# Optimization experiments

Measured on AMD Instinct MI355X. Metric: run time of the kernel, lower is better.

The kernel has to match this reference:

```python
import jax, jax.numpy as jnp
import numpy as np

B, D, C, OUT = 16384, 784, 2048, 10

def setup_inputs() -> dict:
    key = jax.random.key(0)
    k1, k2, k3 = jax.random.split(key, 3)
    x = jax.random.normal(k1, (B, D), dtype=jnp.float32)
    centres = jax.random.normal(k2, (C, D), dtype=jnp.float32)
    log_sigmas = jnp.zeros((C,), dtype=jnp.float32)
    W = jax.random.normal(k3, (OUT, C), dtype=jnp.float32) * (1.0 / np.sqrt(C))
    b = jnp.zeros((OUT,), dtype=jnp.float32)
    return {"x": x, "centres": centres, "log_sigmas": log_sigmas, "W": W, "b": b}

def reference(x, centres, log_sigmas, W, b):
    # (B, C, D) broadcast tensor the torch code materializes; same math).
    x2 = jnp.sum(x * x, axis=-1, keepdims=True)          # (B, 1)
    c2 = jnp.sum(centres * centres, axis=-1)             # (C,)
    d2 = jnp.maximum(x2 + c2[None, :] - 2.0 * (x @ centres.T), 0.0)  # (B, C)
    distances = jnp.sqrt(d2) / jnp.exp(log_sigmas)[None, :]          # (B, C)
    phi = jnp.exp(-(distances * distances))              # gaussian basis
    return phi @ W.T + b                                  # (B, OUT)
```

## Files before the change

kernel.cpp:

```cpp
#include <hip/hip_runtime.h>


#define B_ROWS 16384
#define D_DIM  784
#define C_DIM  2048
#define NOUT   10
#define KPAD   832
#define NT32   26

typedef __attribute__((ext_vector_type(8))) __bf16 bf16x8;
typedef __attribute__((ext_vector_type(4))) float  f32x4;
typedef __attribute__((ext_vector_type(4))) unsigned short ushort4v;

__device__ __forceinline__ unsigned short f2bf(float f) {
  union { float f; unsigned int u; } v; v.f = f;
  unsigned int u = v.u;
  return (unsigned short)((u + 0x7fffu + ((u >> 16) & 1u)) >> 16);
}

__device__ __forceinline__ void async16(const unsigned short* g, unsigned short* l) {
  __builtin_amdgcn_global_load_lds((const __attribute__((address_space(1))) void*)g,
                                   (__attribute__((address_space(3))) void*)l,
                                   16, 0, 0);
}

__device__ __forceinline__ void conv_row(const float* __restrict__ src,
                                         unsigned short* __restrict__ dst,
                                         float* __restrict__ sq, int row, int lane) {
  const float* s = src + (size_t)row * D_DIM;
  unsigned short* d = dst + (size_t)row * KPAD;
  float acc = 0.f;
#pragma unroll
  for (int c = 0; c < 4; ++c) {
    const int ch = lane + c * 64;
    if (ch < 196) {
      const float4 v = ((const float4*)s)[ch];
      ushort4v o; o.x = f2bf(v.x); o.y = f2bf(v.y); o.z = f2bf(v.z); o.w = f2bf(v.w);
      *(ushort4v*)(d + ch * 4) = o;
      acc += v.x * v.x + v.y * v.y + v.z * v.z + v.w * v.w;
    } else if (ch < 208) {
      ushort4v z = {0, 0, 0, 0};
      *(ushort4v*)(d + ch * 4) = z;
    }
  }
#pragma unroll
  for (int off = 32; off > 0; off >>= 1) acc += __shfl_down(acc, off);
  if (lane == 0) sq[row] = acc;
}

__global__ __launch_bounds__(256) void prep_all(
    const float* __restrict__ x, const float* __restrict__ cen,
    const float* __restrict__ ls, const float* __restrict__ W,
    const float* __restrict__ bias,
    unsigned short* __restrict__ xb, unsigned short* __restrict__ cb,
    unsigned short* __restrict__ wb,
    float* __restrict__ x2, float* __restrict__ c2, float* __restrict__ sc,
    float* __restrict__ out) {
  const int bx = blockIdx.x;
  if (bx < B_ROWS / 4) {
    conv_row(x, xb, x2, bx * 4 + (threadIdx.x >> 6), threadIdx.x & 63);
  } else if (bx < B_ROWS / 4 + C_DIM / 4) {
    conv_row(cen, cb, c2, (bx - B_ROWS / 4) * 4 + (threadIdx.x >> 6), threadIdx.x & 63);
  } else {
    const int i = (bx - (B_ROWS / 4 + C_DIM / 4)) * 256 + threadIdx.x;
    if (i < B_ROWS * NOUT) out[i] = bias[i % NOUT];
    const int j = i - B_ROWS * NOUT;
    if (j >= 0 && j < 16 * C_DIM)
      wb[j] = ((j >> 11) < NOUT) ? f2bf(W[(j >> 11) * C_DIM + (j & 2047)]) : (unsigned short)0;
    const int k = j - 16 * C_DIM;
    if (k >= 0 && k < C_DIM) sc[k] = __expf(-2.f * ls[k]);
  }
}

__global__ __launch_bounds__(512, 2) void rbf_main(
    const unsigned short* __restrict__ xb, const unsigned short* __restrict__ cb,
    const unsigned short* __restrict__ wb,
    const float* __restrict__ x2, const float* __restrict__ c2,
    const float* __restrict__ scale, float* __restrict__ out) {
  __shared__ __align__(16) char smem[138240];
  unsigned short* Ph = (unsigned short*)smem;
  float* x2s = (float*)(smem + 135168);
  float* c2s = (float*)(smem + 136192);
  float* scs = (float*)(smem + 137216);

  const int tid  = threadIdx.x;
  const int w    = tid >> 6;
  const int lane = tid & 63;
  const int q    = lane >> 4;
  const int l16  = lane & 15;
  const int brow = blockIdx.x * 256;
  const int bcol = blockIdx.y * 256;
  const int wr   = (w >> 2) * 128;
  const int wc   = (w & 3) * 64;

  if (tid < 256) { c2s[tid] = c2[bcol + tid]; scs[tid] = scale[bcol + tid]; }
  else           { x2s[tid - 256] = x2[brow + tid - 256]; }
  asm volatile("s_waitcnt vmcnt(0)" ::: "memory");

  const int srow = tid >> 2;
  const int soct = (tid & 3) ^ (srow & 3);
  const unsigned short* sA = xb + (size_t)(brow + srow) * KPAD + soct * 8;
  const unsigned short* sB = cb + (size_t)(bcol + srow) * KPAD + soct * 8;
  const int wslot = w * 512;

#define STG(T) { unsigned short* bb = (unsigned short*)(smem + ((T) & 3) * 32768); \
    const int k0_ = (T) * 32;                                                      \
    async16(sA + k0_,              bb         + wslot);                            \
    async16(sA + 128*KPAD + k0_,   bb + 4096  + wslot);                            \
    async16(sB + k0_,              bb + 8192  + wslot);                            \
    async16(sB + 128*KPAD + k0_,   bb + 12288 + wslot); }

  STG(0); STG(1); STG(2);

  f32x4 acc[8][4] = {};
  const int osw = (q ^ (l16 & 3)) << 3;

  for (int t = 0; t < NT32; ++t) {
    if (t < NT32 - 2)       asm volatile("s_waitcnt vmcnt(8)" ::: "memory");
    else if (t == NT32 - 2) asm volatile("s_waitcnt vmcnt(4)" ::: "memory");
    else                    asm volatile("s_waitcnt vmcnt(0)" ::: "memory");
    __builtin_amdgcn_s_barrier();

    if (t < NT32 - 3) STG(t + 3);

    const unsigned short* As = (const unsigned short*)(smem + (t & 3) * 32768);
    const unsigned short* Bs = As + 8192;
    bf16x8 af[8], bfr[4];
#pragma unroll
    for (int i = 0; i < 8; ++i)
      af[i] = *(const bf16x8*)&As[(wr + i * 16 + l16) * 32 + osw];
#pragma unroll
    for (int j = 0; j < 4; ++j)
      bfr[j] = *(const bf16x8*)&Bs[(wc + j * 16 + l16) * 32 + osw];
    __builtin_amdgcn_s_setprio(1);
#pragma unroll
    for (int i = 0; i < 8; ++i)
#pragma unroll
      for (int j = 0; j < 4; ++j)
        acc[i][j] = __builtin_amdgcn_mfma_f32_16x16x32_bf16(af[i], bfr[j], acc[i][j], 0, 0, 0);
    __builtin_amdgcn_s_setprio(0);
  }
#undef STG

  __syncthreads();

#pragma unroll
  for (int i = 0; i < 8; ++i) {
#pragma unroll
    for (int j = 0; j < 4; ++j) {
      const int cl = wc + j * 16 + l16;
      const float c2v = c2s[cl];
      const float sc = scs[cl];
#pragma unroll
      for (int r = 0; r < 4; ++r) {
        const int rl = wr + i * 16 + q * 4 + r;
        float d2 = fmaxf(x2s[rl] + c2v - 2.f * acc[i][j][r], 0.f);
        Ph[rl * 264 + cl] = f2bf(__expf(-d2 * sc));
      }
    }
  }
  __syncthreads();

  f32x4 oacc[2] = {};
#pragma unroll
  for (int kk = 0; kk < 8; ++kk) {
    const bf16x8 bw = *(const bf16x8*)&wb[(size_t)l16 * C_DIM + bcol + kk * 32 + q * 8];
#pragma unroll
    for (int mi = 0; mi < 2; ++mi) {
      const bf16x8 ap = *(const bf16x8*)&Ph[(w * 32 + mi * 16 + l16) * 264 + kk * 32 + q * 8];
      oacc[mi] = __builtin_amdgcn_mfma_f32_16x16x32_bf16(ap, bw, oacc[mi], 0, 0, 0);
    }
  }
  if (l16 < NOUT) {
#pragma unroll
    for (int mi = 0; mi < 2; ++mi)
#pragma unroll
      for (int r = 0; r < 4; ++r) {
        const int grow = brow + w * 32 + mi * 16 + q * 4 + r;
        atomicAdd(&out[grow * NOUT + l16], oacc[mi][r]);
      }
  }
}

extern "C" void kernel_launch(void* const* d_in, const int* in_sizes, int n_in,
                              void* d_out, int out_size, void* d_ws, size_t ws_size,
                              hipStream_t stream) {
  const float* x    = (const float*)d_in[0];
  const float* cen  = (const float*)d_in[1];
  const float* ls   = (const float*)d_in[2];
  const float* W    = (const float*)d_in[3];
  const float* bias = (const float*)d_in[4];
  float* out = (float*)d_out;

  unsigned char* ws = (unsigned char*)d_ws;
  unsigned short* xb  = (unsigned short*)(ws);
  unsigned short* cbf = (unsigned short*)(ws + 27262976);
  unsigned short* wb  = (unsigned short*)(ws + 30670848);
  float* x2 = (float*)(ws + 30736384);
  float* c2 = (float*)(ws + 30801920);
  float* sc = (float*)(ws + 30810112);

  const int prep_blocks = B_ROWS / 4 + C_DIM / 4 +
                          (B_ROWS * NOUT + 16 * C_DIM + C_DIM + 255) / 256;
  prep_all<<<prep_blocks, 256, 0, stream>>>(x, cen, ls, W, bias, xb, cbf, wb, x2, c2, sc, out);
  rbf_main<<<dim3(B_ROWS / 256, C_DIM / 256), 512, 0, stream>>>(xb, cbf, wb, x2, c2, sc, out);
}
```

Measured before the change: 167.0 us.

## Double the K tile to 64 and use a two-stage double-buffered LDS pipeline

The main GEMM loop now stages K=64 slices instead of K=32, cutting the loop to 13 iterations and halving the number of barriers and waitcnts. The four-buffer ring with three slices in flight becomes a two-buffer scheme that prefetches only the next slice. An XOR swizzle over eight 16-byte chunks keeps LDS reads conflict-free with the wider rows. In exchange, prefetch depth drops from three slices to one, so global-load latency is less hidden behind MFMA work.

```diff
diff --git a/kernel.cpp b/kernel.cpp
--- a/kernel.cpp
+++ b/kernel.cpp
@@ -6,7 +6,8 @@
 #define C_DIM  2048
 #define NOUT   10
 #define KPAD   832
-#define NT32   26
+#define BK     64
+#define NT     13
 
 typedef __attribute__((ext_vector_type(8))) __bf16 bf16x8;
 typedef __attribute__((ext_vector_type(4))) float  f32x4;
@@ -88,6 +89,7 @@
   const int lane = tid & 63;
   const int q    = lane >> 4;
   const int l16  = lane & 15;
+  const int swz  = l16 & 7;
   const int brow = blockIdx.x * 256;
   const int bcol = blockIdx.y * 256;
   const int wr   = (w >> 2) * 128;
@@ -97,48 +99,62 @@
   else           { x2s[tid - 256] = x2[brow + tid - 256]; }
   asm volatile("s_waitcnt vmcnt(0)" ::: "memory");
 
-  const int srow = tid >> 2;
-  const int soct = (tid & 3) ^ (srow & 3);
-  const unsigned short* sA = xb + (size_t)(brow + srow) * KPAD + soct * 8;
-  const unsigned short* sB = cb + (size_t)(bcol + srow) * KPAD + soct * 8;
-  const int wslot = w * 512;
-
-#define STG(T) { unsigned short* bb = (unsigned short*)(smem + ((T) & 3) * 32768); \
-    const int k0_ = (T) * 32;                                                      \
-    async16(sA + k0_,              bb         + wslot);                            \
-    async16(sA + 128*KPAD + k0_,   bb + 4096  + wslot);                            \
-    async16(sB + k0_,              bb + 8192  + wslot);                            \
-    async16(sB + 128*KPAD + k0_,   bb + 12288 + wslot); }
-
-  STG(0); STG(1); STG(2);
+  const int srow = tid >> 3;
+  const int skc  = (tid & 7) ^ (srow & 7);
+  const unsigned short* gA = xb + (size_t)(brow + srow) * KPAD + skc * 8;
+  const unsigned short* gB = cb + (size_t)(bcol + srow) * KPAD + skc * 8;
+  const int ldst = w * 512;
+
+#define STG(T) { unsigned short* bbA = (unsigned short*)(smem + ((T) & 1) * 65536);   \
+    unsigned short* bbB = bbA + 16384;                                                \
+    const int k0_ = (T) * BK;                                                         \
+    async16(gA + k0_,                bbA         + ldst);                             \
+    async16(gA + (size_t)64*KPAD  + k0_, bbA + 4096  + ldst);                         \
+    async16(gA + (size_t)128*KPAD + k0_, bbA + 8192  + ldst);                         \
+    async16(gA + (size_t)192*KPAD + k0_, bbA + 12288 + ldst);                         \
+    async16(gB + k0_,                bbB         + ldst);                             \
+    async16(gB + (size_t)64*KPAD  + k0_, bbB + 4096  + ldst);                         \
+    async16(gB + (size_t)128*KPAD + k0_, bbB + 8192  + ldst);                         \
+    async16(gB + (size_t)192*KPAD + k0_, bbB + 12288 + ldst); }
+
+  STG(0); STG(1);
 
   f32x4 acc[8][4] = {};
-  const int osw = (q ^ (l16 & 3)) << 3;
-
-  for (int t = 0; t < NT32; ++t) {
-    if (t < NT32 - 2)       asm volatile("s_waitcnt vmcnt(8)" ::: "memory");
-    else if (t == NT32 - 2) asm volatile("s_waitcnt vmcnt(4)" ::: "memory");
-    else                    asm volatile("s_waitcnt vmcnt(0)" ::: "memory");
+
+  for (int t = 0; t < NT; ++t) {
+    if (t == 0) asm volatile("s_waitcnt vmcnt(8)" ::: "memory");
+    else        asm volatile("s_waitcnt vmcnt(0)" ::: "memory");
     __builtin_amdgcn_s_barrier();
 
-    if (t < NT32 - 3) STG(t + 3);
-
-    const unsigned short* As = (const unsigned short*)(smem + (t & 3) * 32768);
-    const unsigned short* Bs = As + 8192;
-    bf16x8 af[8], bfr[4];
-#pragma unroll
-    for (int i = 0; i < 8; ++i)
-      af[i] = *(const bf16x8*)&As[(wr + i * 16 + l16) * 32 + osw];
-#pragma unroll
-    for (int j = 0; j < 4; ++j)
-      bfr[j] = *(const bf16x8*)&Bs[(wc + j * 16 + l16) * 32 + osw];
-    __builtin_amdgcn_s_setprio(1);
-#pragma unroll
-    for (int i = 0; i < 8; ++i)
+    if (t >= 1 && t < NT - 1) STG(t + 1);
+
+    const unsigned short* As = (const unsigned short*)(smem + (t & 1) * 65536);
+    const unsigned short* Bs = As + 16384;
+    bf16x8 af0[4], af1[4], bfr[4];
+#pragma unroll
+    for (int ks = 0; ks < 2; ++ks) {
 #pragma unroll
       for (int j = 0; j < 4; ++j)
-        acc[i][j] = __builtin_amdgcn_mfma_f32_16x16x32_bf16(af[i], bfr[j], acc[i][j], 0, 0, 0);
-    __builtin_amdgcn_s_setprio(0);
+        bfr[j] = *(const bf16x8*)&Bs[(wc + j * 16 + l16) * 64 + (((ks * 4 + q) ^ swz) << 3)];
+#pragma unroll
+      for (int ii = 0; ii < 4; ++ii)
+        af0[ii] = *(const bf16x8*)&As[(wr + ii * 16 + l16) * 64 + (((ks * 4 + q) ^ swz) << 3)];
+#pragma unroll
+      for (int ii = 0; ii < 4; ++ii)
+        af1[ii] = *(const bf16x8*)&As[(wr + 64 + ii * 16 + l16) * 64 + (((ks * 4 + q) ^ swz) << 3)];
+      __builtin_amdgcn_s_setprio(1);
+#pragma unroll
+      for (int ii = 0; ii < 4; ++ii)
+#pragma unroll
+        for (int j = 0; j < 4; ++j)
+          acc[ii][j] = __builtin_amdgcn_mfma_f32_16x16x32_bf16(af0[ii], bfr[j], acc[ii][j], 0, 0, 0);
+#pragma unroll
+      for (int ii = 0; ii < 4; ++ii)
+#pragma unroll
+        for (int j = 0; j < 4; ++j)
+          acc[4 + ii][j] = __builtin_amdgcn_mfma_f32_16x16x32_bf16(af1[ii], bfr[j], acc[4 + ii][j], 0, 0, 0);
+      __builtin_amdgcn_s_setprio(0);
+    }
   }
 #undef STG
 
```

Result: faster. 160.6 us (-3.8%).

## Replace LDS-staged GEMM pipeline with direct global-to-register double-buffered loads and smaller tiles

Applied to the files above, without the earlier changes.

Drops the async global-to-LDS four-stage pipeline and its barriers. Each wave now loads its MFMA fragments directly from global memory into registers, double-buffered across k-steps. The block tile shrinks from 256x256 with 8 waves to 128x128 with 4 waves, and LDS is only used for the phi tile, which lets more blocks fit per CU. The trade-off is that operands are no longer shared through LDS, so redundant global/L2 traffic rises and the fragment loads are strided per row. Atomic output adds also double because there are more column blocks.

```diff
diff --git a/kernel.cpp b/kernel.cpp
--- a/kernel.cpp
+++ b/kernel.cpp
@@ -6,7 +6,7 @@
 #define C_DIM  2048
 #define NOUT   10
 #define KPAD   832
-#define NT32   26
+#define NSTEP  26
 
 typedef __attribute__((ext_vector_type(8))) __bf16 bf16x8;
 typedef __attribute__((ext_vector_type(4))) float  f32x4;
@@ -16,12 +16,6 @@
   union { float f; unsigned int u; } v; v.f = f;
   unsigned int u = v.u;
   return (unsigned short)((u + 0x7fffu + ((u >> 16) & 1u)) >> 16);
-}
-
-__device__ __forceinline__ void async16(const unsigned short* g, unsigned short* l) {
-  __builtin_amdgcn_global_load_lds((const __attribute__((address_space(1))) void*)g,
-                                   (__attribute__((address_space(3))) void*)l,
-                                   16, 0, 0);
 }
 
 __device__ __forceinline__ void conv_row(const float* __restrict__ src,
@@ -72,80 +66,72 @@
   }
 }
 
-__global__ __launch_bounds__(512, 2) void rbf_main(
+__global__ __launch_bounds__(256, 3) void rbf_main(
     const unsigned short* __restrict__ xb, const unsigned short* __restrict__ cb,
     const unsigned short* __restrict__ wb,
     const float* __restrict__ x2, const float* __restrict__ c2,
     const float* __restrict__ scale, float* __restrict__ out) {
-  __shared__ __align__(16) char smem[138240];
+  __shared__ __align__(16) char smem[34816];
   unsigned short* Ph = (unsigned short*)smem;
-  float* x2s = (float*)(smem + 135168);
-  float* c2s = (float*)(smem + 136192);
-  float* scs = (float*)(smem + 137216);
+  __shared__ float x2s[128], c2s[128], scs[128];
 
   const int tid  = threadIdx.x;
   const int w    = tid >> 6;
   const int lane = tid & 63;
   const int q    = lane >> 4;
   const int l16  = lane & 15;
-  const int brow = blockIdx.x * 256;
-  const int bcol = blockIdx.y * 256;
-  const int wr   = (w >> 2) * 128;
-  const int wc   = (w & 3) * 64;
+  const int brow = blockIdx.x * 128;
+  const int bcol = blockIdx.y * 128;
+  const int wr   = (w >> 1) * 64;
+  const int wc   = (w & 1) * 64;
 
-  if (tid < 256) { c2s[tid] = c2[bcol + tid]; scs[tid] = scale[bcol + tid]; }
-  else           { x2s[tid - 256] = x2[brow + tid - 256]; }
-  asm volatile("s_waitcnt vmcnt(0)" ::: "memory");
+  if (tid < 128) x2s[tid] = x2[brow + tid];
+  else { c2s[tid - 128] = c2[bcol + tid - 128]; scs[tid - 128] = scale[bcol + tid - 128]; }
 
-  const int srow = tid >> 2;
-  const int soct = (tid & 3) ^ (srow & 3);
-  const unsigned short* sA = xb + (size_t)(brow + srow) * KPAD + soct * 8;
-  const unsigned short* sB = cb + (size_t)(bcol + srow) * KPAD + soct * 8;
-  const int wslot = w * 512;
+  const unsigned short* pA[4];
+  const unsigned short* pB[4];
+#pragma unroll
+  for (int i = 0; i < 4; ++i) {
+    pA[i] = xb + (size_t)(brow + wr + i * 16 + l16) * KPAD + q * 8;
+    pB[i] = cb + (size_t)(bcol + wc + i * 16 + l16) * KPAD + q * 8;
+  }
 
-#define STG(T) { unsigned short* bb = (unsigned short*)(smem + ((T) & 3) * 32768); \
-    const int k0_ = (T) * 32;                                                      \
-    async16(sA + k0_,              bb         + wslot);                            \
-    async16(sA + 128*KPAD + k0_,   bb + 4096  + wslot);                            \
-    async16(sB + k0_,              bb + 8192  + wslot);                            \
-    async16(sB + 128*KPAD + k0_,   bb + 12288 + wslot); }
+#define LDSET(A_, B_, S)                                                    \
+  _Pragma("unroll")                                                         \
+  for (int ii = 0; ii < 4; ++ii) A_[ii] = *(const bf16x8*)(pA[ii] + (S) * 32); \
+  _Pragma("unroll")                                                         \
+  for (int jj = 0; jj < 4; ++jj) B_[jj] = *(const bf16x8*)(pB[jj] + (S) * 32);
 
-  STG(0); STG(1); STG(2);
+#define MFMA16(A_, B_)                                                      \
+  _Pragma("unroll")                                                         \
+  for (int ii = 0; ii < 4; ++ii)                                            \
+    _Pragma("unroll")                                                       \
+    for (int jj = 0; jj < 4; ++jj)                                          \
+      acc[ii][jj] = __builtin_amdgcn_mfma_f32_16x16x32_bf16(                \
+          A_[ii], B_[jj], acc[ii][jj], 0, 0, 0);
 
-  f32x4 acc[8][4] = {};
-  const int osw = (q ^ (l16 & 3)) << 3;
+  f32x4 acc[4][4] = {};
+  bf16x8 a0[4], b0[4], a1[4], b1[4];
 
-  for (int t = 0; t < NT32; ++t) {
-    if (t < NT32 - 2)       asm volatile("s_waitcnt vmcnt(8)" ::: "memory");
-    else if (t == NT32 - 2) asm volatile("s_waitcnt vmcnt(4)" ::: "memory");
-    else                    asm volatile("s_waitcnt vmcnt(0)" ::: "memory");
-    __builtin_amdgcn_s_barrier();
-
-    if (t < NT32 - 3) STG(t + 3);
-
-    const unsigned short* As = (const unsigned short*)(smem + (t & 3) * 32768);
-    const unsigned short* Bs = As + 8192;
-    bf16x8 af[8], bfr[4];
+  LDSET(a0, b0, 0)
+  LDSET(a1, b1, 1)
 #pragma unroll
-    for (int i = 0; i < 8; ++i)
-      af[i] = *(const bf16x8*)&As[(wr + i * 16 + l16) * 32 + osw];
-#pragma unroll
-    for (int j = 0; j < 4; ++j)
-      bfr[j] = *(const bf16x8*)&Bs[(wc + j * 16 + l16) * 32 + osw];
-    __builtin_amdgcn_s_setprio(1);
-#pragma unroll
-    for (int i = 0; i < 8; ++i)
-#pragma unroll
-      for (int j = 0; j < 4; ++j)
-        acc[i][j] = __builtin_amdgcn_mfma_f32_16x16x32_bf16(af[i], bfr[j], acc[i][j], 0, 0, 0);
-    __builtin_amdgcn_s_setprio(0);
+  for (int s = 0; s < NSTEP; ++s) {
+    if ((s & 1) == 0) {
+      MFMA16(a0, b0)
+      if (s + 2 < NSTEP) { LDSET(a0, b0, s + 2) }
+    } else {
+      MFMA16(a1, b1)
+      if (s + 2 < NSTEP) { LDSET(a1, b1, s + 2) }
+    }
   }
-#undef STG
+#undef LDSET
+#undef MFMA16
 
   __syncthreads();
 
 #pragma unroll
-  for (int i = 0; i < 8; ++i) {
+  for (int i = 0; i < 4; ++i) {
 #pragma unroll
     for (int j = 0; j < 4; ++j) {
       const int cl = wc + j * 16 + l16;
@@ -155,7 +141,7 @@
       for (int r = 0; r < 4; ++r) {
         const int rl = wr + i * 16 + q * 4 + r;
         float d2 = fmaxf(x2s[rl] + c2v - 2.f * acc[i][j][r], 0.f);
-        Ph[rl * 264 + cl] = f2bf(__expf(-d2 * sc));
+        Ph[rl * 136 + cl] = f2bf(__expf(-d2 * sc));
       }
     }
   }
@@ -163,11 +149,11 @@
 
   f32x4 oacc[2] = {};
 #pragma unroll
-  for (int kk = 0; kk < 8; ++kk) {
+  for (int kk = 0; kk < 4; ++kk) {
     const bf16x8 bw = *(const bf16x8*)&wb[(size_t)l16 * C_DIM + bcol + kk * 32 + q * 8];
 #pragma unroll
     for (int mi = 0; mi < 2; ++mi) {
-      const bf16x8 ap = *(const bf16x8*)&Ph[(w * 32 + mi * 16 + l16) * 264 + kk * 32 + q * 8];
+      const bf16x8 ap = *(const bf16x8*)&Ph[(w * 32 + mi * 16 + l16) * 136 + kk * 32 + q * 8];
       oacc[mi] = __builtin_amdgcn_mfma_f32_16x16x32_bf16(ap, bw, oacc[mi], 0, 0, 0);
     }
   }
@@ -203,5 +189,5 @@
   const int prep_blocks = B_ROWS / 4 + C_DIM / 4 +
                           (B_ROWS * NOUT + 16 * C_DIM + C_DIM + 255) / 256;
   prep_all<<<prep_blocks, 256, 0, stream>>>(x, cen, ls, W, bias, xb, cbf, wb, x2, c2, sc, out);
-  rbf_main<<<dim3(B_ROWS / 256, C_DIM / 256), 512, 0, stream>>>(xb, cbf, wb, x2, c2, sc, out);
+  rbf_main<<<dim3(B_ROWS / 128, C_DIM / 128), 256, 0, stream>>>(xb, cbf, wb, x2, c2, sc, out);
 }
```

Result: slower. 290.5 us (+74.0%).
